# Kernel tuning notes

Measured on AMD Instinct MI355X. Metric: run time of the kernel, lower is better.

Reference implementation:

```python
import jax, jax.numpy as jnp
import numpy as np

TEMPERATURE = 0.07
LOG_EPS = 1e-20
MEAN_EPS = 1e-6


def setup_inputs() -> dict:
    key = jax.random.key(0)
    k1, k2, k3 = jax.random.split(key, 3)
    B, T1, I1, C = 64, 33, 197, 512  # 1+seqlen=33, 1+14*14=197
    text_embeds = jax.random.normal(k1, (B, T1, C), dtype=jnp.float32)
    video_embeds = jax.random.normal(k2, (B, I1, C), dtype=jnp.float32)
    text_attn_mask = jax.random.randint(k3, (B, T1), 0, 2).astype(jnp.int32)
    # guarantee every row has at least one attended (non-CLS) token
    text_attn_mask = text_attn_mask.at[:, :2].set(1)
    return {"text_embeds": text_embeds, "video_embeds": video_embeds,
            "text_attn_mask": text_attn_mask}


def reference(text_embeds, video_embeds, text_attn_mask):
    # NOTE: original normalizes over dim=1 (sequence axis), kept faithfully.
    te = text_embeds / jnp.linalg.norm(text_embeds, axis=1, keepdims=True)
    ve = video_embeds / jnp.linalg.norm(video_embeds, axis=1, keepdims=True)
    mask = text_attn_mask[:, 1:].astype(bool)          # [B, T] (trim CLS)
    text_latents = te[:, 1:, :]                        # [B, T, C]
    # full late-interaction score tensor, scaled (multiplied) by temperature
    sim = jnp.einsum('xtd,yid->xyti', text_latents, ve) * TEMPERATURE  # [X,Y,T,I]

    # text -> image: max over image tokens, masked mean over text tokens
    t2i = sim.max(axis=-1)                             # [X, Y, T]
    m = mask[None, :, None, :]                         # [1, B, 1, T] (X must == B)
    numer = jnp.where(m, t2i[None], 0.0).sum(axis=-1)  # [1, B, Y]
    denom = jnp.maximum(mask.sum(axis=-1).astype(sim.dtype), MEAN_EPS)[None, :, None]
    text_to_image = numer / denom                      # [1, B, Y]

    # image -> text: masked max over text tokens, mean over image tokens
    # (computed in the original module but unused in the returned loss)
    m5 = mask[None, :, None, :, None]                  # [1, B, 1, T, 1]
    neg = -jnp.finfo(sim.dtype).max
    image_to_text = jnp.where(m5, sim[None], neg).max(axis=-2).mean(axis=-1)  # [1,B,Y]
    del image_to_text  # dead in original: loss = text_to_image_loss only

    t2i_exp = jnp.exp(text_to_image)                   # [1, B, Y]
    pos = jnp.diagonal(t2i_exp, axis1=-2, axis2=-1)    # [1, min(B, Y)]
    den = t2i_exp.sum(axis=-1)                         # [1, B]
    loss = -jnp.log(pos / den + LOG_EPS).mean(axis=-1)  # [1]
    return loss
```

## Files before the change

kernel.cpp:

```cpp
#include <hip/hip_runtime.h>
#include <hip/hip_bf16.h>
#include <float.h>
#include <math.h>

#define BB 64
#define T1 33
#define TT 32
#define II 197
#define CC 512
#define TEMP 0.07f

typedef float f32x4 __attribute__((ext_vector_type(4)));
typedef int i32x4 __attribute__((ext_vector_type(4)));
typedef int i32x8 __attribute__((ext_vector_type(8)));

#define TL_OFF  0
#define VE_OFF  (1 << 20)
#define TTI_OFF ((1 << 20) + (8 << 20))
#define KS_STRIDE   32768
#define GRP_STRIDE  131072

__global__ __launch_bounds__(512) void norm_all_kernel(const float* __restrict__ text,
                                                       const float* __restrict__ video,
                                                       unsigned char* __restrict__ tl8,
                                                       unsigned char* __restrict__ ve8) {
  int b = blockIdx.x, hz = blockIdx.y, tid = threadIdx.x;
  bool isV = hz < 4;
  int h2 = isV ? hz : hz - 4;
  const float* src = isV ? (video + (size_t)b * II * CC) : (text + (size_t)b * T1 * CC);
  int n = isV ? II : T1;

  __shared__ float cache[II][132];
  __shared__ float red[16][128];
  __shared__ float rn[128];

  {
    int c4 = tid & 31, rg = tid >> 5;
    const float* p = src + h2 * 128 + c4 * 4;
    float4 s = {0.f, 0.f, 0.f, 0.f};
    for (int i = rg; i < n; i += 16) {
      float4 v = *(const float4*)(p + (size_t)i * CC);
      *(float4*)&cache[i][c4 * 4] = v;
      s.x += v.x * v.x; s.y += v.y * v.y; s.z += v.z * v.z; s.w += v.w * v.w;
    }
    *(float4*)&red[rg][c4 * 4] = s;
  }
  __syncthreads();
  if (tid < 128) {
    float s = 0.f;
#pragma unroll
    for (int g = 0; g < 16; ++g) s += red[g][tid];
    rn[tid] = 1.0f / sqrtf(s);
  }
  __syncthreads();

  if (isV) {
    for (int S = tid; S < 13 * 128; S += 512) {
      int fb = S >> 7, h = (S >> 6) & 1, lane = S & 63;
      int i = fb * 16 + (lane & 15);
      int kloc = ((lane >> 4) & 3) * 32 + h * 16;
      unsigned int wd[4];
#pragma unroll
      for (int q = 0; q < 4; ++q) {
        f32x4 u = {0.f, 0.f, 0.f, 0.f};
        if (i < II) u = *(const f32x4*)&cache[i][kloc + q * 4];
        f32x4 r = *(const f32x4*)&rn[kloc + q * 4];
        int wv = __builtin_amdgcn_cvt_pk_fp8_f32(u[0] * r[0], u[1] * r[1], 0, 0);
        wv = __builtin_amdgcn_cvt_pk_fp8_f32(u[2] * r[2], u[3] * r[3], wv, 1);
        wd[q] = (unsigned int)wv;
      }
      unsigned char* dst = ve8 + (size_t)b * GRP_STRIDE + h2 * KS_STRIDE +
                           fb * 2048 + h * 1024 + lane * 16;
      *(uint4*)dst = make_uint4(wd[0], wd[1], wd[2], wd[3]);
    }
  } else if (tid < 256) {
    int fa_local = tid >> 7, h = (tid >> 6) & 1, lane = tid & 63;
    int t = fa_local * 16 + (lane & 15);
    int kloc = ((lane >> 4) & 3) * 32 + h * 16;
    unsigned int wd[4];
#pragma unroll
    for (int q = 0; q < 4; ++q) {
      f32x4 u = *(const f32x4*)&cache[1 + t][kloc + q * 4];
      f32x4 r = *(const f32x4*)&rn[kloc + q * 4];
      int wv = __builtin_amdgcn_cvt_pk_fp8_f32(u[0] * r[0], u[1] * r[1], 0, 0);
      wv = __builtin_amdgcn_cvt_pk_fp8_f32(u[2] * r[2], u[3] * r[3], wv, 1);
      wd[q] = (unsigned int)wv;
    }
    int fa = (b & 7) * 2 + fa_local;
    unsigned char* dst = tl8 + (size_t)(b >> 3) * GRP_STRIDE + h2 * KS_STRIDE +
                         fa * 2048 + h * 1024 + lane * 16;
    *(uint4*)dst = make_uint4(wd[0], wd[1], wd[2], wd[3]);
  }
}

typedef __attribute__((address_space(3))) unsigned int lds_u32;
typedef __attribute__((address_space(1))) const unsigned int glb_u32;
__device__ __forceinline__ void gl16(const unsigned char* g, unsigned char* l) {
  __builtin_amdgcn_global_load_lds((glb_u32*)(const void*)g, (lds_u32*)(void*)l, 16, 0, 0);
}

__global__ __launch_bounds__(512, 2) void sim_kernel(const unsigned char* __restrict__ tl8,
                                                     const unsigned char* __restrict__ ve8,
                                                     const int* __restrict__ mask,
                                                     float* __restrict__ tti) {
  int L = blockIdx.x;
  int xcd = L & 7;
  int idx = L >> 3;
  int y = xcd * 8 + (idx & 7);
  int xcb = idx >> 3;

  int tid = threadIdx.x;
  int w = tid >> 6, lane = tid & 63;
  int wm = w >> 2;
  int wn = w & 3;

  __shared__ __attribute__((aligned(16))) unsigned char As[3][8 * 2048];
  __shared__ __attribute__((aligned(16))) unsigned char Bs[3][16 * 2048];
  __shared__ float smax[4 * 128];

  const unsigned char* Abase =
      tl8 + (size_t)(xcb >> 1) * GRP_STRIDE + (size_t)(xcb & 1) * 8 * 2048;
  const unsigned char* Bbase = ve8 + (size_t)y * GRP_STRIDE;

#define STG(s_) do {                                                          \
    int slot_ = (s_) % 3;                                                     \
    _Pragma("unroll")                                                         \
    for (int r_ = 0; r_ < 6; ++r_) {                                          \
      int g_ = w * 6 + r_;                                                    \
      if (g_ < 16) {                                                          \
        int fa_ = g_ >> 1, h_ = g_ & 1;                                       \
        const unsigned char* src_ =                                           \
            Abase + (size_t)(s_) * KS_STRIDE + fa_ * 2048 + h_ * 1024 + lane * 16; \
        gl16(src_, &As[slot_][(fa_ * 2 + h_) * 1024 + lane * 16]);            \
      } else {                                                                \
        int gb_ = g_ - 16;                                                    \
        int fb_ = gb_ >> 1, h_ = gb_ & 1;                                     \
        const unsigned char* src_ =                                           \
            Bbase + (size_t)(s_) * KS_STRIDE + fb_ * 2048 + h_ * 1024 + lane * 16; \
        gl16(src_, &Bs[slot_][(fb_ * 2 + h_) * 1024 + lane * 16]);            \
      }                                                                       \
    }                                                                         \
  } while (0)

#define KCOMPUTE(slot_, NF_) do {                                             \
    i32x8 aop_[4];                                                            \
    _Pragma("unroll")                                                         \
    for (int ma_ = 0; ma_ < 4; ++ma_) {                                       \
      i32x4 h0_ = *(const i32x4*)&As[slot_][((wm * 4 + ma_) * 2) * 1024 + lane * 16]; \
      i32x4 h1_ = *(const i32x4*)&As[slot_][((wm * 4 + ma_) * 2 + 1) * 1024 + lane * 16]; \
      aop_[ma_] = __builtin_shufflevector(h0_, h1_, 0, 1, 2, 3, 4, 5, 6, 7);  \
    }                                                                         \
    i32x8 bop_[NF_];                                                          \
    _Pragma("unroll")                                                         \
    for (int nb_ = 0; nb_ < NF_; ++nb_) {                                     \
      int fb_ = wn + 4 * nb_;                                                 \
      i32x4 h0_ = *(const i32x4*)&Bs[slot_][(fb_ * 2) * 1024 + lane * 16];    \
      i32x4 h1_ = *(const i32x4*)&Bs[slot_][(fb_ * 2 + 1) * 1024 + lane * 16]; \
      bop_[nb_] = __builtin_shufflevector(h0_, h1_, 0, 1, 2, 3, 4, 5, 6, 7);  \
    }                                                                         \
    __builtin_amdgcn_s_setprio(1);                                            \
    _Pragma("unroll")                                                         \
    for (int ma_ = 0; ma_ < 4; ++ma_)                                         \
      _Pragma("unroll")                                                       \
      for (int nb_ = 0; nb_ < NF_; ++nb_)                                     \
        acc[ma_][nb_] = __builtin_amdgcn_mfma_scale_f32_16x16x128_f8f6f4(     \
            aop_[ma_], bop_[nb_], acc[ma_][nb_], 0, 0,                        \
            0, 0x7F7F7F7F, 0, 0x7F7F7F7F);                                    \
    __builtin_amdgcn_s_setprio(0);                                            \
  } while (0)

  f32x4 acc[4][4] = {};

  STG(0); STG(1);
  asm volatile("s_waitcnt vmcnt(6)" ::: "memory");
  __builtin_amdgcn_s_barrier();

  STG(2);
  if (wn == 0) KCOMPUTE(0, 4); else KCOMPUTE(0, 3);
  asm volatile("s_waitcnt vmcnt(6)" ::: "memory");
  __builtin_amdgcn_s_barrier();
  STG(3);
  if (wn == 0) KCOMPUTE(1, 4); else KCOMPUTE(1, 3);
  asm volatile("s_waitcnt vmcnt(6)" ::: "memory");
  __builtin_amdgcn_s_barrier();
  if (wn == 0) KCOMPUTE(2, 4); else KCOMPUTE(2, 3);
  asm volatile("s_waitcnt vmcnt(0)" ::: "memory");
  __builtin_amdgcn_s_barrier();
  if (wn == 0) KCOMPUTE(0, 4); else KCOMPUTE(0, 3);
#undef STG
#undef KCOMPUTE

  int col = lane & 15, gq = lane >> 4;
  int nfrag = (wn == 0) ? 4 : 3;
  bool valid[4];
#pragma unroll
  for (int nb = 0; nb < 4; ++nb) {
    int fb = wn + 4 * nb;
    valid[nb] = (nb < nfrag) && (fb * 16 + col < II);
  }

  float mx[4][4];
#pragma unroll
  for (int ma = 0; ma < 4; ++ma)
#pragma unroll
    for (int reg = 0; reg < 4; ++reg) {
      float m = -FLT_MAX;
#pragma unroll
      for (int nb = 0; nb < 4; ++nb)
        if (valid[nb]) m = fmaxf(m, acc[ma][nb][reg]);
      mx[ma][reg] = m;
    }
#pragma unroll
  for (int st = 1; st <= 8; st <<= 1)
#pragma unroll
    for (int ma = 0; ma < 4; ++ma)
#pragma unroll
      for (int reg = 0; reg < 4; ++reg)
        mx[ma][reg] = fmaxf(mx[ma][reg], __shfl_xor(mx[ma][reg], st));

  if (col == 0) {
#pragma unroll
    for (int ma = 0; ma < 4; ++ma)
#pragma unroll
      for (int reg = 0; reg < 4; ++reg)
        smax[wn * 128 + wm * 64 + ma * 16 + gq * 4 + reg] = mx[ma][reg];
  }
  __syncthreads();

  if (tid < 128) {
    int r = tid;
    float m = fmaxf(fmaxf(smax[r], smax[128 + r]),
                    fmaxf(smax[256 + r], smax[384 + r]));
    int x = xcb * 4 + (r >> 5), tt = r & 31;
    int mk = mask[x * T1 + 1 + tt];
    float num = mk ? m * TEMP : 0.f;
    float cnt = mk ? 1.f : 0.f;
#pragma unroll
    for (int st = 1; st < 32; st <<= 1) {
      num += __shfl_xor(num, st);
      cnt += __shfl_xor(cnt, st);
    }
    if (tt == 0) tti[x * 64 + y] = num / fmaxf(cnt, 1e-6f);
  }
}

__global__ void loss_kernel(const float* __restrict__ tti, float* __restrict__ out) {
  __shared__ float lxs[64];
  int tid = threadIdx.x;
  int x = tid >> 4, q = tid & 15;
  float4 v = *(const float4*)&tti[x * 64 + q * 4];
  float den = expf(v.x) + expf(v.y) + expf(v.z) + expf(v.w);
#pragma unroll
  for (int st = 1; st < 16; st <<= 1) den += __shfl_xor(den, st);
  if (q == 0) {
    float pos = expf(tti[x * 64 + x]);
    lxs[x] = -logf(pos / den + 1e-20f);
  }
  __syncthreads();
  if (tid < 64) {
    float lx = lxs[tid];
#pragma unroll
    for (int s = 1; s < 64; s <<= 1) lx += __shfl_xor(lx, s);
    if (tid == 0) out[0] = lx * (1.0f / 64.0f);
  }
}

extern "C" void kernel_launch(void* const* d_in, const int* in_sizes, int n_in,
                              void* d_out, int out_size, void* d_ws, size_t ws_size,
                              hipStream_t stream) {
  const float* text = (const float*)d_in[0];
  const float* video = (const float*)d_in[1];
  const int* mask = (const int*)d_in[2];
  float* out = (float*)d_out;

  char* ws = (char*)d_ws;
  unsigned char* tl8 = (unsigned char*)(ws + TL_OFF);
  unsigned char* ve8 = (unsigned char*)(ws + VE_OFF);
  float* tti = (float*)(ws + TTI_OFF);

  hipLaunchKernelGGL(norm_all_kernel, dim3(BB, 8), dim3(512), 0, stream, text, video, tl8, ve8);
  hipLaunchKernelGGL(sim_kernel, dim3(1024), dim3(512), 0, stream, tl8, ve8, mask, tti);
  hipLaunchKernelGGL(loss_kernel, dim3(1), dim3(1024), 0, stream, tti, out);
}
```

Before: 45.97 us.

## Shrink LDS to double buffer and load 13th B fragment from global for 4 blocks/CU

Result: slower. 70.80 us (+54.0%).

```diff
diff --git a/kernel.cpp b/kernel.cpp
--- a/kernel.cpp
+++ b/kernel.cpp
@@ -99,7 +99,7 @@
   __builtin_amdgcn_global_load_lds((glb_u32*)(const void*)g, (lds_u32*)(void*)l, 16, 0, 0);
 }
 
-__global__ __launch_bounds__(512, 2) void sim_kernel(const unsigned char* __restrict__ tl8,
+__global__ __launch_bounds__(512, 4) void sim_kernel(const unsigned char* __restrict__ tl8,
                                                      const unsigned char* __restrict__ ve8,
                                                      const int* __restrict__ mask,
                                                      float* __restrict__ tti) {
@@ -114,19 +114,19 @@
   int wm = w >> 2;
   int wn = w & 3;
 
-  __shared__ __attribute__((aligned(16))) unsigned char As[3][8 * 2048];
-  __shared__ __attribute__((aligned(16))) unsigned char Bs[3][16 * 2048];
-  __shared__ float smax[4 * 128];
+  __shared__ __attribute__((aligned(16))) unsigned char As[2][8 * 2048];
+  __shared__ __attribute__((aligned(16))) unsigned char Bs[2][12 * 2048];
+  float* smax = (float*)&As[0][0];
 
   const unsigned char* Abase =
       tl8 + (size_t)(xcb >> 1) * GRP_STRIDE + (size_t)(xcb & 1) * 8 * 2048;
   const unsigned char* Bbase = ve8 + (size_t)y * GRP_STRIDE;
 
 #define STG(s_) do {                                                          \
-    int slot_ = (s_) % 3;                                                     \
+    int slot_ = (s_) & 1;                                                     \
     _Pragma("unroll")                                                         \
-    for (int r_ = 0; r_ < 6; ++r_) {                                          \
-      int g_ = w * 6 + r_;                                                    \
+    for (int r_ = 0; r_ < 5; ++r_) {                                          \
+      int g_ = w * 5 + r_;                                                    \
       if (g_ < 16) {                                                          \
         int fa_ = g_ >> 1, h_ = g_ & 1;                                       \
         const unsigned char* src_ =                                           \
@@ -142,7 +142,14 @@
     }                                                                         \
   } while (0)
 
-#define KCOMPUTE(slot_, NF_) do {                                             \
+#define KCOMPUTE(slot_, s_, F12_) do {                                        \
+    i32x4 g0_ = {0, 0, 0, 0}, g1_ = {0, 0, 0, 0};                             \
+    if (F12_) {                                                               \
+      const unsigned char* p_ =                                               \
+          Bbase + (size_t)(s_) * KS_STRIDE + 12 * 2048 + lane * 16;           \
+      g0_ = *(const i32x4*)p_;                                                \
+      g1_ = *(const i32x4*)(p_ + 1024);                                       \
+    }                                                                         \
     i32x8 aop_[4];                                                            \
     _Pragma("unroll")                                                         \
     for (int ma_ = 0; ma_ < 4; ++ma_) {                                       \
@@ -150,43 +157,49 @@
       i32x4 h1_ = *(const i32x4*)&As[slot_][((wm * 4 + ma_) * 2 + 1) * 1024 + lane * 16]; \
       aop_[ma_] = __builtin_shufflevector(h0_, h1_, 0, 1, 2, 3, 4, 5, 6, 7);  \
     }                                                                         \
-    i32x8 bop_[NF_];                                                          \
+    __builtin_amdgcn_s_setprio(1);                                            \
     _Pragma("unroll")                                                         \
-    for (int nb_ = 0; nb_ < NF_; ++nb_) {                                     \
+    for (int nb_ = 0; nb_ < 3; ++nb_) {                                       \
       int fb_ = wn + 4 * nb_;                                                 \
       i32x4 h0_ = *(const i32x4*)&Bs[slot_][(fb_ * 2) * 1024 + lane * 16];    \
       i32x4 h1_ = *(const i32x4*)&Bs[slot_][(fb_ * 2 + 1) * 1024 + lane * 16]; \
-      bop_[nb_] = __builtin_shufflevector(h0_, h1_, 0, 1, 2, 3, 4, 5, 6, 7);  \
-    }                                                                         \
-    __builtin_amdgcn_s_setprio(1);                                            \
-    _Pragma("unroll")                                                         \
-    for (int ma_ = 0; ma_ < 4; ++ma_)                                         \
+      i32x8 bop_ = __builtin_shufflevector(h0_, h1_, 0, 1, 2, 3, 4, 5, 6, 7); \
       _Pragma("unroll")                                                       \
-      for (int nb_ = 0; nb_ < NF_; ++nb_)                                     \
+      for (int ma_ = 0; ma_ < 4; ++ma_)                                       \
         acc[ma_][nb_] = __builtin_amdgcn_mfma_scale_f32_16x16x128_f8f6f4(     \
-            aop_[ma_], bop_[nb_], acc[ma_][nb_], 0, 0,                        \
+            aop_[ma_], bop_, acc[ma_][nb_], 0, 0,                             \
             0, 0x7F7F7F7F, 0, 0x7F7F7F7F);                                    \
+    }                                                                         \
+    if (F12_) {                                                               \
+      i32x8 bop_ = __builtin_shufflevector(g0_, g1_, 0, 1, 2, 3, 4, 5, 6, 7); \
+      _Pragma("unroll")                                                       \
+      for (int ma_ = 0; ma_ < 4; ++ma_)                                       \
+        acc[ma_][3] = __builtin_amdgcn_mfma_scale_f32_16x16x128_f8f6f4(       \
+            aop_[ma_], bop_, acc[ma_][3], 0, 0,                               \
+            0, 0x7F7F7F7F, 0, 0x7F7F7F7F);                                    \
+    }                                                                         \
     __builtin_amdgcn_s_setprio(0);                                            \
   } while (0)
 
   f32x4 acc[4][4] = {};
 
-  STG(0); STG(1);
-  asm volatile("s_waitcnt vmcnt(6)" ::: "memory");
-  __builtin_amdgcn_s_barrier();
-
+  STG(0);
+  asm volatile("s_waitcnt vmcnt(0)" ::: "memory");
+  __builtin_amdgcn_s_barrier();
+
+  STG(1);
+  if (wn == 0) KCOMPUTE(0, 0, 1); else KCOMPUTE(0, 0, 0);
+  asm volatile("s_waitcnt vmcnt(0)" ::: "memory");
+  __builtin_amdgcn_s_barrier();
   STG(2);
-  if (wn == 0) KCOMPUTE(0, 4); else KCOMPUTE(0, 3);
-  asm volatile("s_waitcnt vmcnt(6)" ::: "memory");
+  if (wn == 0) KCOMPUTE(1, 1, 1); else KCOMPUTE(1, 1, 0);
+  asm volatile("s_waitcnt vmcnt(0)" ::: "memory");
   __builtin_amdgcn_s_barrier();
   STG(3);
-  if (wn == 0) KCOMPUTE(1, 4); else KCOMPUTE(1, 3);
-  asm volatile("s_waitcnt vmcnt(6)" ::: "memory");
-  __builtin_amdgcn_s_barrier();
-  if (wn == 0) KCOMPUTE(2, 4); else KCOMPUTE(2, 3);
-  asm volatile("s_waitcnt vmcnt(0)" ::: "memory");
-  __builtin_amdgcn_s_barrier();
-  if (wn == 0) KCOMPUTE(0, 4); else KCOMPUTE(0, 3);
+  if (wn == 0) KCOMPUTE(0, 2, 1); else KCOMPUTE(0, 2, 0);
+  asm volatile("s_waitcnt vmcnt(0)" ::: "memory");
+  __builtin_amdgcn_s_barrier();
+  if (wn == 0) KCOMPUTE(1, 3, 1); else KCOMPUTE(1, 3, 0);
 #undef STG
 #undef KCOMPUTE
 
@@ -218,6 +231,7 @@
       for (int reg = 0; reg < 4; ++reg)
         mx[ma][reg] = fmaxf(mx[ma][reg], __shfl_xor(mx[ma][reg], st));
 
+  __syncthreads();
   if (col == 0) {
 #pragma unroll
     for (int ma = 0; ma < 4; ++ma)
```
